# Performance work log

Measured on AMD Instinct MI355X. Metric: run time of the kernel, lower is better.

Reference implementation:

```python
import jax, jax.numpy as jnp
import numpy as np

ALPHA = 0.0257
DELTA_T = 3.0
SOURCE_INTENSITY = 100000.0
MASK_THRESHOLD = 1000.0


def _laplace_kernel():
    # 7-point 3D Laplacian stencil, shape [O=1, I=1, 3, 3, 3]
    k = np.zeros((1, 1, 3, 3, 3), dtype=np.float32)
    k[0, 0, 1, 1, 1] = -6.0
    k[0, 0, 0, 1, 1] = 1.0
    k[0, 0, 2, 1, 1] = 1.0
    k[0, 0, 1, 0, 1] = 1.0
    k[0, 0, 1, 2, 1] = 1.0
    k[0, 0, 1, 1, 0] = 1.0
    k[0, 0, 1, 1, 2] = 1.0
    return jnp.asarray(k)


def setup_inputs() -> dict:
    key = jax.random.key(0)
    k1, k2 = jax.random.split(key)
    shape = (8, 1, 128, 128, 128)  # [B, C=1, D, H, W]
    model_output = jax.random.normal(k1, shape, dtype=jnp.float32)
    current_input = jax.random.normal(k2, shape, dtype=jnp.float32)
    return {"model_output": model_output, "current_input": current_input}


def reference(model_output, current_input):
    kernel = _laplace_kernel().astype(current_input.dtype)
    # zero-padded 3x3x3 depthwise (C=1) Laplacian stencil
    laplacian = jax.lax.conv_general_dilated(
        current_input, kernel,
        window_strides=(1, 1, 1),
        padding=[(1, 1), (1, 1), (1, 1)],
        dimension_numbers=("NCDHW", "OIDHW", "NCDHW"),
    )
    temporal_derivative = (model_output - current_input) / DELTA_T
    source_term = jnp.where(current_input > MASK_THRESHOLD,
                            jnp.asarray(SOURCE_INTENSITY, current_input.dtype),
                            jnp.asarray(0.0, current_input.dtype))
    residual = temporal_derivative - ALPHA * laplacian - source_term
    return jnp.mean(residual * residual)
```

## Files before the change

kernel.cpp:

```cpp
#include <hip/hip_runtime.h>


constexpr int WW = 128;
constexpr int HH = 128;
constexpr int DD = 128;
constexpr long long N_ELEM = 8LL * DD * HH * WW;
constexpr int NBLOCKS = 2048;

constexpr float ALPHA  = 0.0257f;
constexpr float INV_DT = 1.0f / 3.0f;
constexpr float SRC_I  = 100000.0f;
constexpr float THRESH = 1000.0f;

__device__ __forceinline__ float sq_residual4(
        const float4 c, const float4 m,
        const float4 ym, const float4 yp,
        const float4 zm, const float4 zp,
        const float fym, const float fyp, const float fzm, const float fzp,
        const bool x_lo, const bool x_hi, float acc) {
    float left  = __shfl_up(c.w, 1, 64);
    float right = __shfl_down(c.x, 1, 64);
    if (x_lo) left = 0.0f;
    if (x_hi) right = 0.0f;

    const float cc[4]  = {c.x, c.y, c.z, c.w};
    const float mm[4]  = {m.x, m.y, m.z, m.w};
    const float xs[6]  = {left, c.x, c.y, c.z, c.w, right};
    const float yms[4] = {ym.x, ym.y, ym.z, ym.w};
    const float yps[4] = {yp.x, yp.y, yp.z, yp.w};
    const float zms[4] = {zm.x, zm.y, zm.z, zm.w};
    const float zps[4] = {zp.x, zp.y, zp.z, zp.w};

    #pragma unroll
    for (int j = 0; j < 4; ++j) {
        float lap = xs[j] + xs[j + 2] - 6.0f * cc[j];
        lap = fmaf(fym, yms[j], lap);
        lap = fmaf(fyp, yps[j], lap);
        lap = fmaf(fzm, zms[j], lap);
        lap = fmaf(fzp, zps[j], lap);
        const float td  = (mm[j] - cc[j]) * INV_DT;
        const float src = (cc[j] > THRESH) ? SRC_I : 0.0f;
        const float r   = td - ALPHA * lap - src;
        acc = fmaf(r, r, acc);
    }
    return acc;
}

__global__ __launch_bounds__(256) void heat_loss_kernel(
        const float* __restrict__ model,
        const float* __restrict__ cur,
        float* __restrict__ block_sums) {
    const int tid = blockIdx.x * blockDim.x + threadIdx.x;
    const int x4 = tid & 31;
    const int y  = (tid >> 5) & 127;
    const int z  = (tid >> 12) & 127;

    const bool x_lo = (x4 == 0);
    const bool x_hi = (x4 == 31);
    const float fym = (y == 0)   ? 0.0f : 1.0f;
    const float fyp = (y == 127) ? 0.0f : 1.0f;
    const float fzm = (z == 0)   ? 0.0f : 1.0f;
    const float fzp = (z == 127) ? 0.0f : 1.0f;
    const int off_ym = (y == 0)   ? 0 : -WW;
    const int off_yp = (y == 127) ? 0 :  WW;
    const int off_zm = (z == 0)   ? 0 : -HH * WW;
    const int off_zp = (z == 127) ? 0 :  HH * WW;

    int i = (z * HH + y) * WW + x4 * 4;

    float acc = 0.0f;

    #pragma unroll 1
    for (int bb = 0; bb < 4; ++bb) {
        const int i0 = i;
        const int i1 = i + (1 << 21);

        const float4 c0  = *reinterpret_cast<const float4*>(cur   + i0);
        const float4 m0  = *reinterpret_cast<const float4*>(model + i0);
        const float4 ym0 = *reinterpret_cast<const float4*>(cur   + i0 + off_ym);
        const float4 yp0 = *reinterpret_cast<const float4*>(cur   + i0 + off_yp);
        const float4 zm0 = *reinterpret_cast<const float4*>(cur   + i0 + off_zm);
        const float4 zp0 = *reinterpret_cast<const float4*>(cur   + i0 + off_zp);
        const float4 c1  = *reinterpret_cast<const float4*>(cur   + i1);
        const float4 m1  = *reinterpret_cast<const float4*>(model + i1);
        const float4 ym1 = *reinterpret_cast<const float4*>(cur   + i1 + off_ym);
        const float4 yp1 = *reinterpret_cast<const float4*>(cur   + i1 + off_yp);
        const float4 zm1 = *reinterpret_cast<const float4*>(cur   + i1 + off_zm);
        const float4 zp1 = *reinterpret_cast<const float4*>(cur   + i1 + off_zp);

        acc = sq_residual4(c0, m0, ym0, yp0, zm0, zp0, fym, fyp, fzm, fzp, x_lo, x_hi, acc);
        acc = sq_residual4(c1, m1, ym1, yp1, zm1, zp1, fym, fyp, fzm, fzp, x_lo, x_hi, acc);

        i += (1 << 22);
    }

    #pragma unroll
    for (int off = 32; off > 0; off >>= 1)
        acc += __shfl_down(acc, off, 64);

    __shared__ float wsum[4];
    const int lane = threadIdx.x & 63;
    const int wave = threadIdx.x >> 6;
    if (lane == 0) wsum[wave] = acc;
    __syncthreads();

    if (threadIdx.x == 0)
        block_sums[blockIdx.x] = wsum[0] + wsum[1] + wsum[2] + wsum[3];
}

__global__ __launch_bounds__(256) void finalize_kernel(
        const float* __restrict__ block_sums, float* __restrict__ out) {
    double a = 0.0;
    for (int j = threadIdx.x; j < NBLOCKS; j += 256)
        a += (double)block_sums[j];

    #pragma unroll
    for (int off = 32; off > 0; off >>= 1)
        a += __shfl_down(a, off, 64);

    __shared__ double wsum[4];
    const int lane = threadIdx.x & 63;
    const int wave = threadIdx.x >> 6;
    if (lane == 0) wsum[wave] = a;
    __syncthreads();

    if (threadIdx.x == 0)
        out[0] = (float)((wsum[0] + wsum[1] + wsum[2] + wsum[3]) / (double)N_ELEM);
}

extern "C" void kernel_launch(void* const* d_in, const int* in_sizes, int n_in,
                              void* d_out, int out_size, void* d_ws, size_t ws_size,
                              hipStream_t stream) {
    const float* model = (const float*)d_in[0];
    const float* cur   = (const float*)d_in[1];
    float* block_sums = (float*)d_ws;
    float* out = (float*)d_out;

    heat_loss_kernel<<<NBLOCKS, 256, 0, stream>>>(model, cur, block_sums);
    finalize_kernel<<<1, 256, 0, stream>>>(block_sums, out);
}
```

Baseline: 146.5 us.

## Stream along z with register-rotated planes and software-prefetched loads

Each block now handles an 8-row y strip for one batch and marches through a 16-plane z chunk. The centre and z-minus values are carried in registers from the previous step instead of being reloaded. The next plane's loads are issued one step ahead, with a sched_barrier to keep them ahead of the compute, and model loads use nontemporal hints. This cuts redundant cur loads and keeps memory in flight, at the cost of more registers and a serial dependency along z within each thread.

```diff
diff --git a/kernel.cpp b/kernel.cpp
--- a/kernel.cpp
+++ b/kernel.cpp
@@ -4,13 +4,38 @@
 constexpr int WW = 128;
 constexpr int HH = 128;
 constexpr int DD = 128;
+constexpr int PLANE = HH * WW;
 constexpr long long N_ELEM = 8LL * DD * HH * WW;
-constexpr int NBLOCKS = 2048;
+constexpr int ZCHUNK = 16;
+constexpr int NBLOCKS = 8 * 16 * (DD / ZCHUNK);
 
 constexpr float ALPHA  = 0.0257f;
 constexpr float INV_DT = 1.0f / 3.0f;
 constexpr float SRC_I  = 100000.0f;
 constexpr float THRESH = 1000.0f;
+
+typedef float f32x4 __attribute__((ext_vector_type(4)));
+
+struct L4 { float4 zp, m, ym, yp; };
+
+__device__ __forceinline__ float4 ldg4(const float* p) {
+    return *reinterpret_cast<const float4*>(p);
+}
+__device__ __forceinline__ float4 ldnt4(const float* p) {
+    f32x4 v = __builtin_nontemporal_load(reinterpret_cast<const f32x4*>(p));
+    return make_float4(v.x, v.y, v.z, v.w);
+}
+
+__device__ __forceinline__ L4 load_step(const float* __restrict__ cur,
+                                        const float* __restrict__ model,
+                                        int i, int ozp, int oym, int oyp) {
+    L4 t;
+    t.zp = ldg4(cur + i + ozp);
+    t.m  = ldnt4(model + i);
+    t.ym = ldg4(cur + i + oym);
+    t.yp = ldg4(cur + i + oyp);
+    return t;
+}
 
 __device__ __forceinline__ float sq_residual4(
         const float4 c, const float4 m,
@@ -50,49 +75,54 @@
         const float* __restrict__ model,
         const float* __restrict__ cur,
         float* __restrict__ block_sums) {
-    const int tid = blockIdx.x * blockDim.x + threadIdx.x;
-    const int x4 = tid & 31;
-    const int y  = (tid >> 5) & 127;
-    const int z  = (tid >> 12) & 127;
+    const int bx = blockIdx.x;
+    const int zc = bx & 7;
+    const int ys = (bx >> 3) & 15;
+    const int b  = bx >> 7;
+    const int z0 = zc * ZCHUNK;
+
+    const int x4 = threadIdx.x & 31;
+    const int yr = threadIdx.x >> 5;
+    const int y  = ys * 8 + yr;
 
     const bool x_lo = (x4 == 0);
     const bool x_hi = (x4 == 31);
     const float fym = (y == 0)   ? 0.0f : 1.0f;
     const float fyp = (y == 127) ? 0.0f : 1.0f;
-    const float fzm = (z == 0)   ? 0.0f : 1.0f;
-    const float fzp = (z == 127) ? 0.0f : 1.0f;
-    const int off_ym = (y == 0)   ? 0 : -WW;
-    const int off_yp = (y == 127) ? 0 :  WW;
-    const int off_zm = (z == 0)   ? 0 : -HH * WW;
-    const int off_zp = (z == 127) ? 0 :  HH * WW;
+    const int oym = (y == 0)   ? 0 : -WW;
+    const int oyp = (y == 127) ? 0 :  WW;
 
-    int i = (z * HH + y) * WW + x4 * 4;
+    int i = ((b * DD + z0) * HH + y) * WW + x4 * 4;
+
+    const int ozm0 = (z0 == 0) ? 0 : -PLANE;
+    float fzm = (z0 == 0) ? 0.0f : 1.0f;
+    float4 zm = ldg4(cur + i + ozm0);
+    float4 c  = ldg4(cur + i);
+
+    L4 t0 = load_step(cur, model, i, PLANE, oym, oyp);
 
     float acc = 0.0f;
 
     #pragma unroll 1
-    for (int bb = 0; bb < 4; ++bb) {
-        const int i0 = i;
-        const int i1 = i + (1 << 21);
+    for (int s = 0; s < ZCHUNK - 1; ++s) {
+        const int zz1 = z0 + s + 1;
+        const int ozp1 = (zz1 == 127) ? 0 : PLANE;
+        L4 t1 = load_step(cur, model, i + PLANE, ozp1, oym, oyp);
 
-        const float4 c0  = *reinterpret_cast<const float4*>(cur   + i0);
-        const float4 m0  = *reinterpret_cast<const float4*>(model + i0);
-        const float4 ym0 = *reinterpret_cast<const float4*>(cur   + i0 + off_ym);
-        const float4 yp0 = *reinterpret_cast<const float4*>(cur   + i0 + off_yp);
-        const float4 zm0 = *reinterpret_cast<const float4*>(cur   + i0 + off_zm);
-        const float4 zp0 = *reinterpret_cast<const float4*>(cur   + i0 + off_zp);
-        const float4 c1  = *reinterpret_cast<const float4*>(cur   + i1);
-        const float4 m1  = *reinterpret_cast<const float4*>(model + i1);
-        const float4 ym1 = *reinterpret_cast<const float4*>(cur   + i1 + off_ym);
-        const float4 yp1 = *reinterpret_cast<const float4*>(cur   + i1 + off_yp);
-        const float4 zm1 = *reinterpret_cast<const float4*>(cur   + i1 + off_zm);
-        const float4 zp1 = *reinterpret_cast<const float4*>(cur   + i1 + off_zp);
+        __builtin_amdgcn_sched_barrier(0);
 
-        acc = sq_residual4(c0, m0, ym0, yp0, zm0, zp0, fym, fyp, fzm, fzp, x_lo, x_hi, acc);
-        acc = sq_residual4(c1, m1, ym1, yp1, zm1, zp1, fym, fyp, fzm, fzp, x_lo, x_hi, acc);
+        acc = sq_residual4(c, t0.m, t0.ym, t0.yp, zm, t0.zp,
+                           fym, fyp, fzm, 1.0f, x_lo, x_hi, acc);
+        zm = c;
+        c  = t0.zp;
+        fzm = 1.0f;
+        t0 = t1;
+        i += PLANE;
+    }
 
-        i += (1 << 22);
-    }
+    const float fzp_last = (z0 + ZCHUNK - 1 == 127) ? 0.0f : 1.0f;
+    acc = sq_residual4(c, t0.m, t0.ym, t0.yp, zm, t0.zp,
+                       fym, fyp, fzm, fzp_last, x_lo, x_hi, acc);
 
     #pragma unroll
     for (int off = 32; off > 0; off >>= 1)
```

Measured after the change: 134.6 us. 1.09x faster.
